# Kernel optimization log

Measured on AMD Instinct MI355X. Metric: run time of the kernel, lower is better.

The kernel has to match this reference:

```python
import jax, jax.numpy as jnp
import numpy as np

B, T, C = 2, 4096, 512
P, PS, CS, MB, FD = 64, 16, 5, 128, 128


def setup_inputs() -> dict:
    key = jax.random.key(0)
    ks = jax.random.split(key, 9)
    y = jax.random.normal(ks[0], (B, T, C), jnp.float32)
    # per-timestep random patch indices into the sequence axis, sorted per patch
    patches = jnp.sort(jax.random.randint(ks[1], (T, P, PS), 0, T), axis=-1).astype(jnp.int32)
    patches_proj = jax.random.randint(ks[2], (T, P), 0, T).astype(jnp.int32)
    W_BASE = jax.random.normal(ks[3], (P, PS, CS), jnp.float32) * 0.05
    W_BIAS = jax.random.normal(ks[4], (P,), jnp.float32) * 0.05
    W_proj2 = jax.random.normal(ks[5], (C, MB), jnp.float32) * (1.0 / np.sqrt(C).astype(np.float32))
    W_proj_comp = jax.random.normal(ks[6], (C, CS), jnp.float32) * (1.0 / np.sqrt(C).astype(np.float32))
    W_presoftmax1 = jax.random.normal(ks[7], (P, P), jnp.float32) * (1.0 / np.sqrt(P).astype(np.float32))
    W_FINAL = jax.random.normal(ks[8], (MB, FD), jnp.float32) * (1.0 / np.sqrt(MB).astype(np.float32))
    return {
        'y': y,
        'W_BASE': W_BASE,
        'W_BIAS': W_BIAS,
        'W_proj2': W_proj2,
        'W_proj_comp': W_proj_comp,
        'W_presoftmax1': W_presoftmax1,
        'W_FINAL': W_FINAL,
        'patches': patches,
        'patches_proj': patches_proj,
    }


def reference(y, W_BASE, W_BIAS, W_proj2, W_proj_comp, W_presoftmax1, W_FINAL, patches, patches_proj):
    # value branch: project then gather one sequence element per (t, patch)
    bm = jnp.einsum('btc,cm->btm', y, W_proj2)          # [B,T,MB]
    mbg = bm[:, patches_proj, :]                        # [B,T,P,MB]  (MBMB)
    # score branch: compress, gather PS elements per (t, patch), weighted reduce
    yc = jnp.einsum('btc,ck->btk', y, W_proj_comp)      # [B,T,CS]
    g = yc[:, patches, :]                               # [B,T,P,PS,CS]
    res = jnp.einsum('btpsc,psc->btp', g, W_BASE) + W_BIAS   # [B,T,P]
    mix = jnp.einsum('btp,pq->btq', res, W_presoftmax1)      # [B,T,P] (no softmax in source)
    out = jnp.einsum('btp,btpm->btm', mix, mbg)              # [B,T,MB]
    return jnp.einsum('btm,mf->btf', out, W_FINAL)           # [B,T,FD]
```

## Files before the change

### kernel.cpp

```cpp
#include <hip/hip_runtime.h>
#include <hip/hip_bf16.h>

#define B_ 2
#define T_ 4096
#define C_ 512
#define P_ 64
#define PS_ 16
#define CS_ 5
#define MB_ 128
#define FD_ 128

using f32x4 = __attribute__((ext_vector_type(4))) float;
using s16x8 = __attribute__((ext_vector_type(8))) short;

static __device__ __forceinline__ float bf_lo(unsigned u) {
  return __uint_as_float(u << 16);
}
static __device__ __forceinline__ float bf_hi(unsigned u) {
  return __uint_as_float(u & 0xffff0000u);
}
static __device__ __forceinline__ float rdlane_f(float v, int p) {
  return __uint_as_float((unsigned)__builtin_amdgcn_readlane((int)__float_as_uint(v), p));
}
static __device__ __forceinline__ ushort bf16u(float f) {
  unsigned x = __float_as_uint(f);
  unsigned r = (x + 0x7fffu + ((x >> 16) & 1u)) >> 16;
  return (ushort)r;
}

__global__ __launch_bounds__(256) void k_cvt(const float* __restrict__ y,
                                             const float* __restrict__ Wc,
                                             ushort* __restrict__ ybf,
                                             ushort* __restrict__ ycp) {
  const int lane = threadIdx.x & 63;
  const int wid  = threadIdx.x >> 6;
  float wc[40];
  {
    const float4* src = (const float4*)(Wc + lane * 40);
    #pragma unroll
    for (int j = 0; j < 10; j++) {
      float4 v = src[j];
      wc[j*4+0] = v.x; wc[j*4+1] = v.y; wc[j*4+2] = v.z; wc[j*4+3] = v.w;
    }
  }
  const int row_base = (blockIdx.x * 4 + wid) * 8;
  #pragma unroll 2
  for (int r = 0; r < 8; r++) {
    const int row = row_base + r;
    const float4* yr = (const float4*)(y + (size_t)row * C_ + lane * 8);
    float4 a = yr[0], b4 = yr[1];
    float e[8] = {a.x, a.y, a.z, a.w, b4.x, b4.y, b4.z, b4.w};
    union { ushort us[8]; uint4 q; } pk;
    #pragma unroll
    for (int j = 0; j < 8; j++) pk.us[j] = bf16u(e[j]);
    *(uint4*)(ybf + (size_t)row * C_ + lane * 8) = pk.q;
    float s0 = 0.f, s1 = 0.f, s2 = 0.f, s3 = 0.f, s4 = 0.f;
    #pragma unroll
    for (int j = 0; j < 8; j++) {
      s0 = fmaf(e[j], wc[j*5+0], s0);
      s1 = fmaf(e[j], wc[j*5+1], s1);
      s2 = fmaf(e[j], wc[j*5+2], s2);
      s3 = fmaf(e[j], wc[j*5+3], s3);
      s4 = fmaf(e[j], wc[j*5+4], s4);
    }
    #pragma unroll
    for (int off = 1; off < 64; off <<= 1) {
      s0 += __shfl_xor(s0, off); s1 += __shfl_xor(s1, off);
      s2 += __shfl_xor(s2, off); s3 += __shfl_xor(s3, off);
      s4 += __shfl_xor(s4, off);
    }
    float myv = (lane == 0) ? s0 : (lane == 1) ? s1 : (lane == 2) ? s2
              : (lane == 3) ? s3 : (lane == 4) ? s4 : 0.f;
    if (lane < 8) ycp[(size_t)row * 8 + lane] = bf16u(myv);
  }
}

__global__ __launch_bounds__(256) void k_cvtW(const float* __restrict__ Wp2,
                                              const float* __restrict__ WF,
                                              ushort* __restrict__ Wp2T,
                                              ushort* __restrict__ WFT) {
  const int id = blockIdx.x * 256 + threadIdx.x;
  if (id < C_ * MB_) {
    const int c = id >> 7, m = id & 127;
    Wp2T[(size_t)m * C_ + c] = bf16u(Wp2[id]);
  }
  const int id2 = id - C_ * MB_;
  if (id2 >= 0 && id2 < MB_ * FD_) {
    const int m = id2 >> 7, f = id2 & 127;
    WFT[(size_t)f * MB_ + m] = bf16u(WF[id2]);
  }
}

template<int KTOT, bool OUTBF>
__global__ __launch_bounds__(256) void k_gemm(const ushort* __restrict__ A,
                                              const ushort* __restrict__ Bt,
                                              void* __restrict__ Cout) {
  __shared__ __align__(16) char smem[(64 + 128) * 128];
  const int tid  = threadIdx.x;
  const int lane = tid & 63;
  const int wid  = tid >> 6;
  const int wm = wid >> 1, wn = wid & 1;
  const int rowA0 = blockIdx.x * 64;

  f32x4 acc[2][4];
  #pragma unroll
  for (int m = 0; m < 2; m++)
    #pragma unroll
    for (int n = 0; n < 4; n++) acc[m][n] = (f32x4){0.f, 0.f, 0.f, 0.f};

  for (int step = 0; step < KTOT / 64; step++) {
    const int kc = step * 64;
    uint4 ra[2], rb[4];
    #pragma unroll
    for (int i = 0; i < 2; i++) {
      const int slot = tid + i * 256, r = slot >> 3, sl = slot & 7;
      ra[i] = *(const uint4*)(A + (size_t)(rowA0 + r) * KTOT + kc + sl * 8);
    }
    #pragma unroll
    for (int i = 0; i < 4; i++) {
      const int slot = tid + i * 256, r = slot >> 3, sl = slot & 7;
      rb[i] = *(const uint4*)(Bt + (size_t)r * KTOT + kc + sl * 8);
    }
    __syncthreads();
    #pragma unroll
    for (int i = 0; i < 2; i++) {
      const int slot = tid + i * 256, r = slot >> 3, sl = slot & 7;
      *(uint4*)(smem + r * 128 + ((sl * 16) ^ ((r & 7) << 4))) = ra[i];
    }
    #pragma unroll
    for (int i = 0; i < 4; i++) {
      const int slot = tid + i * 256, r = slot >> 3, sl = slot & 7;
      *(uint4*)(smem + 8192 + r * 128 + ((sl * 16) ^ ((r & 7) << 4))) = rb[i];
    }
    __syncthreads();
    #pragma unroll
    for (int kk = 0; kk < 2; kk++) {
      const int cb = kk * 64 + (lane >> 4) * 16;
      s16x8 a[2], b[4];
      #pragma unroll
      for (int m = 0; m < 2; m++) {
        const int r = wm * 32 + m * 16 + (lane & 15);
        a[m] = *(const s16x8*)(smem + r * 128 + (cb ^ ((r & 7) << 4)));
      }
      #pragma unroll
      for (int n = 0; n < 4; n++) {
        const int rn = wn * 64 + n * 16 + (lane & 15);
        b[n] = *(const s16x8*)(smem + 8192 + rn * 128 + (cb ^ ((rn & 7) << 4)));
      }
      #pragma unroll
      for (int m = 0; m < 2; m++)
        #pragma unroll
        for (int n = 0; n < 4; n++)
          acc[m][n] = __builtin_amdgcn_mfma_f32_16x16x32_bf16(a[m], b[n], acc[m][n], 0, 0, 0);
    }
  }
  #pragma unroll
  for (int m = 0; m < 2; m++) {
    #pragma unroll
    for (int n = 0; n < 4; n++) {
      #pragma unroll
      for (int reg = 0; reg < 4; reg++) {
        const int grow = rowA0 + wm * 32 + m * 16 + (lane >> 4) * 4 + reg;
        const int gcol = wn * 64 + n * 16 + (lane & 15);
        if (OUTBF)
          ((ushort*)Cout)[(size_t)grow * 128 + gcol] = bf16u(acc[m][n][reg]);
        else
          ((float*)Cout)[(size_t)grow * 128 + gcol] = acc[m][n][reg];
      }
    }
  }
}

__global__ __launch_bounds__(256, 2) void k_mid(
    const ushort* __restrict__ ycp,
    const ushort* __restrict__ bmb,
    const float* __restrict__ WB,
    const float* __restrict__ Wbias,
    const float* __restrict__ Wps1,
    const int* __restrict__ patches,
    const int* __restrict__ pproj,
    ushort* __restrict__ obmb)
{
  const int lane = threadIdx.x & 63;
  const int wid  = threadIdx.x >> 6;
  const int gw   = blockIdx.x * 4 + wid;

  float wb[80];
  {
    const float4* src = (const float4*)(WB + lane * 80);
    #pragma unroll
    for (int j = 0; j < 20; j++) {
      float4 v = src[j];
      wb[j*4+0] = v.x; wb[j*4+1] = v.y; wb[j*4+2] = v.z; wb[j*4+3] = v.w;
    }
  }
  const float bias = Wbias[lane];
  float wcol[64];
  #pragma unroll
  for (int p = 0; p < 64; p++) wcol[p] = Wps1[p * 64 + lane];

  #pragma unroll 1
  for (int tt = 0; tt < 2; tt++) {
    const int t = gw * 2 + tt;
    int idx[16];
    {
      const int4* psrc = (const int4*)(patches + (size_t)t * P_ * PS_ + lane * PS_);
      #pragma unroll
      for (int j = 0; j < 4; j++) {
        int4 v = psrc[j];
        idx[j*4+0] = v.x; idx[j*4+1] = v.y; idx[j*4+2] = v.z; idx[j*4+3] = v.w;
      }
    }
    const int pp = pproj[(size_t)t * P_ + lane];

    #pragma unroll 1
    for (int b = 0; b < B_; b++) {
      const ushort* yb = ycp + (size_t)b * T_ * 8;
      float sum = bias;
      #pragma unroll
      for (int s = 0; s < 16; s++) {
        uint4 g = *(const uint4*)(yb + (size_t)idx[s] * 8);
        sum = fmaf(bf_lo(g.x), wb[s*5+0], sum);
        sum = fmaf(bf_hi(g.x), wb[s*5+1], sum);
        sum = fmaf(bf_lo(g.y), wb[s*5+2], sum);
        sum = fmaf(bf_hi(g.y), wb[s*5+3], sum);
        sum = fmaf(bf_lo(g.z), wb[s*5+4], sum);
      }
      float mix = 0.f;
      #pragma unroll
      for (int p = 0; p < 64; p++)
        mix = fmaf(rdlane_f(sum, p), wcol[p], mix);
      const ushort* bb = bmb + (size_t)b * T_ * MB_;
      float ox = 0.f, oy = 0.f;
      #pragma unroll
      for (int p = 0; p < 64; p++) {
        const float mp = rdlane_f(mix, p);
        const int row = __builtin_amdgcn_readlane(pp, p);
        unsigned v = *(const unsigned*)(bb + (size_t)row * MB_ + lane * 2);
        ox = fmaf(bf_lo(v), mp, ox);
        oy = fmaf(bf_hi(v), mp, oy);
      }
      unsigned pkd = (unsigned)bf16u(ox) | ((unsigned)bf16u(oy) << 16);
      *(unsigned*)(obmb + ((size_t)b * T_ + t) * MB_ + lane * 2) = pkd;
    }
  }
}

extern "C" void kernel_launch(void* const* d_in, const int* in_sizes, int n_in,
                              void* d_out, int out_size, void* d_ws, size_t ws_size,
                              hipStream_t stream) {
  const float* y     = (const float*)d_in[0];
  const float* WB    = (const float*)d_in[1];
  const float* Wbias = (const float*)d_in[2];
  const float* Wp2   = (const float*)d_in[3];
  const float* Wpc   = (const float*)d_in[4];
  const float* Wps1  = (const float*)d_in[5];
  const float* WF    = (const float*)d_in[6];
  const int* patches = (const int*)d_in[7];
  const int* pproj   = (const int*)d_in[8];
  float* out = (float*)d_out;

  char* ws = (char*)d_ws;
  ushort* ybf  = (ushort*)(ws);
  ushort* obmb = (ushort*)(ws);
  ushort* bmb  = (ushort*)(ws + 8388608);
  ushort* ycp  = (ushort*)(ws + 10485760);
  ushort* Wp2T = (ushort*)(ws + 10616832);
  ushort* WFT  = (ushort*)(ws + 10747904);

  k_cvtW<<<dim3(320), dim3(256), 0, stream>>>(Wp2, WF, Wp2T, WFT);
  k_cvt <<<dim3(256), dim3(256), 0, stream>>>(y, Wpc, ybf, ycp);
  k_gemm<512, true> <<<dim3(128), dim3(256), 0, stream>>>(ybf, Wp2T, (void*)bmb);
  k_mid <<<dim3(512), dim3(256), 0, stream>>>(ycp, bmb, WB, Wbias, Wps1,
                                              patches, pproj, obmb);
  k_gemm<128, false><<<dim3(128), dim3(256), 0, stream>>>(obmb, WFT, (void*)out);
}
```

Measured before the change: 151.1 us.

## Fuse weight conversion into prep kernel, convert y inside GEMM, shrink GEMM tiles

Merges the weight-conversion kernel into the y-compression kernel, dropping one launch. The bf16 copy of y is no longer written; the first GEMM reads fp32 y and converts it in registers. Both GEMMs now use 32x64 tiles over 512 blocks instead of 64x128 over 128 blocks, to fill more CUs. In the middle kernel, W_BASE is stored as bf16 and the serial FMA chains are split into multiple accumulators for more ILP. The costs are that every column block reads and converts y again, and W_BASE now carries bf16 precision loss.

```diff
diff --git a/kernel.cpp b/kernel.cpp
--- a/kernel.cpp
+++ b/kernel.cpp
@@ -28,12 +28,35 @@
   return (ushort)r;
 }
 
-__global__ __launch_bounds__(256) void k_cvt(const float* __restrict__ y,
-                                             const float* __restrict__ Wc,
-                                             ushort* __restrict__ ybf,
-                                             ushort* __restrict__ ycp) {
-  const int lane = threadIdx.x & 63;
-  const int wid  = threadIdx.x >> 6;
+__global__ __launch_bounds__(256) void k_prep(const float* __restrict__ y,
+                                              const float* __restrict__ Wc,
+                                              const float* __restrict__ Wp2,
+                                              const float* __restrict__ WF,
+                                              const float* __restrict__ WB,
+                                              ushort* __restrict__ ycp,
+                                              ushort* __restrict__ Wp2T,
+                                              ushort* __restrict__ WFT,
+                                              ushort* __restrict__ WBb) {
+  const int bx = blockIdx.x;
+  const int tid = threadIdx.x;
+  if (bx >= 256) {
+    for (int id = (bx - 256) * 256 + tid; id < 87040; id += 64 * 256) {
+      if (id < 65536) {
+        const int c = id >> 7, m = id & 127;
+        Wp2T[(size_t)m * C_ + c] = bf16u(Wp2[id]);
+      } else if (id < 81920) {
+        const int i2 = id - 65536;
+        const int m = i2 >> 7, f = i2 & 127;
+        WFT[(size_t)f * MB_ + m] = bf16u(WF[i2]);
+      } else {
+        const int i3 = id - 81920;
+        WBb[i3] = bf16u(WB[i3]);
+      }
+    }
+    return;
+  }
+  const int lane = tid & 63;
+  const int wid  = tid >> 6;
   float wc[40];
   {
     const float4* src = (const float4*)(Wc + lane * 40);
@@ -43,17 +66,13 @@
       wc[j*4+0] = v.x; wc[j*4+1] = v.y; wc[j*4+2] = v.z; wc[j*4+3] = v.w;
     }
   }
-  const int row_base = (blockIdx.x * 4 + wid) * 8;
+  const int row_base = (bx * 4 + wid) * 8;
   #pragma unroll 2
   for (int r = 0; r < 8; r++) {
     const int row = row_base + r;
     const float4* yr = (const float4*)(y + (size_t)row * C_ + lane * 8);
     float4 a = yr[0], b4 = yr[1];
     float e[8] = {a.x, a.y, a.z, a.w, b4.x, b4.y, b4.z, b4.w};
-    union { ushort us[8]; uint4 q; } pk;
-    #pragma unroll
-    for (int j = 0; j < 8; j++) pk.us[j] = bf16u(e[j]);
-    *(uint4*)(ybf + (size_t)row * C_ + lane * 8) = pk.q;
     float s0 = 0.f, s1 = 0.f, s2 = 0.f, s3 = 0.f, s4 = 0.f;
     #pragma unroll
     for (int j = 0; j < 8; j++) {
@@ -75,98 +94,82 @@
   }
 }
 
-__global__ __launch_bounds__(256) void k_cvtW(const float* __restrict__ Wp2,
-                                              const float* __restrict__ WF,
-                                              ushort* __restrict__ Wp2T,
-                                              ushort* __restrict__ WFT) {
-  const int id = blockIdx.x * 256 + threadIdx.x;
-  if (id < C_ * MB_) {
-    const int c = id >> 7, m = id & 127;
-    Wp2T[(size_t)m * C_ + c] = bf16u(Wp2[id]);
-  }
-  const int id2 = id - C_ * MB_;
-  if (id2 >= 0 && id2 < MB_ * FD_) {
-    const int m = id2 >> 7, f = id2 & 127;
-    WFT[(size_t)f * MB_ + m] = bf16u(WF[id2]);
-  }
-}
-
-template<int KTOT, bool OUTBF>
-__global__ __launch_bounds__(256) void k_gemm(const ushort* __restrict__ A,
+template<int KTOT, bool OUTBF, bool A_F32>
+__global__ __launch_bounds__(256) void k_gemm(const void* __restrict__ Asrc,
                                               const ushort* __restrict__ Bt,
                                               void* __restrict__ Cout) {
-  __shared__ __align__(16) char smem[(64 + 128) * 128];
+  __shared__ __align__(16) char smem[(32 + 64) * 128];
   const int tid  = threadIdx.x;
   const int lane = tid & 63;
   const int wid  = tid >> 6;
   const int wm = wid >> 1, wn = wid & 1;
-  const int rowA0 = blockIdx.x * 64;
-
-  f32x4 acc[2][4];
-  #pragma unroll
-  for (int m = 0; m < 2; m++)
-    #pragma unroll
-    for (int n = 0; n < 4; n++) acc[m][n] = (f32x4){0.f, 0.f, 0.f, 0.f};
+  const int rowA0 = (blockIdx.x >> 1) * 32;
+  const int bn    = blockIdx.x & 1;
+
+  f32x4 acc[2];
+  acc[0] = (f32x4){0.f, 0.f, 0.f, 0.f};
+  acc[1] = (f32x4){0.f, 0.f, 0.f, 0.f};
 
   for (int step = 0; step < KTOT / 64; step++) {
     const int kc = step * 64;
-    uint4 ra[2], rb[4];
+    uint4 ra;
+    {
+      const int r = tid >> 3, sl = tid & 7;
+      if (A_F32) {
+        const float4* ap = (const float4*)((const float*)Asrc +
+                            (size_t)(rowA0 + r) * KTOT + kc + sl * 8);
+        float4 f0 = ap[0], f1 = ap[1];
+        union { ushort us[8]; uint4 q; } pk;
+        pk.us[0] = bf16u(f0.x); pk.us[1] = bf16u(f0.y);
+        pk.us[2] = bf16u(f0.z); pk.us[3] = bf16u(f0.w);
+        pk.us[4] = bf16u(f1.x); pk.us[5] = bf16u(f1.y);
+        pk.us[6] = bf16u(f1.z); pk.us[7] = bf16u(f1.w);
+        ra = pk.q;
+      } else {
+        ra = *(const uint4*)((const ushort*)Asrc +
+                             (size_t)(rowA0 + r) * KTOT + kc + sl * 8);
+      }
+    }
+    uint4 rb[2];
     #pragma unroll
     for (int i = 0; i < 2; i++) {
       const int slot = tid + i * 256, r = slot >> 3, sl = slot & 7;
-      ra[i] = *(const uint4*)(A + (size_t)(rowA0 + r) * KTOT + kc + sl * 8);
-    }
-    #pragma unroll
-    for (int i = 0; i < 4; i++) {
-      const int slot = tid + i * 256, r = slot >> 3, sl = slot & 7;
-      rb[i] = *(const uint4*)(Bt + (size_t)r * KTOT + kc + sl * 8);
+      rb[i] = *(const uint4*)(Bt + (size_t)(bn * 64 + r) * KTOT + kc + sl * 8);
     }
     __syncthreads();
+    {
+      const int r = tid >> 3, sl = tid & 7;
+      *(uint4*)(smem + r * 128 + ((sl * 16) ^ ((r & 7) << 4))) = ra;
+    }
     #pragma unroll
     for (int i = 0; i < 2; i++) {
       const int slot = tid + i * 256, r = slot >> 3, sl = slot & 7;
-      *(uint4*)(smem + r * 128 + ((sl * 16) ^ ((r & 7) << 4))) = ra[i];
-    }
-    #pragma unroll
-    for (int i = 0; i < 4; i++) {
-      const int slot = tid + i * 256, r = slot >> 3, sl = slot & 7;
-      *(uint4*)(smem + 8192 + r * 128 + ((sl * 16) ^ ((r & 7) << 4))) = rb[i];
+      *(uint4*)(smem + 4096 + r * 128 + ((sl * 16) ^ ((r & 7) << 4))) = rb[i];
     }
     __syncthreads();
     #pragma unroll
     for (int kk = 0; kk < 2; kk++) {
       const int cb = kk * 64 + (lane >> 4) * 16;
-      s16x8 a[2], b[4];
-      #pragma unroll
-      for (int m = 0; m < 2; m++) {
-        const int r = wm * 32 + m * 16 + (lane & 15);
-        a[m] = *(const s16x8*)(smem + r * 128 + (cb ^ ((r & 7) << 4)));
-      }
-      #pragma unroll
-      for (int n = 0; n < 4; n++) {
-        const int rn = wn * 64 + n * 16 + (lane & 15);
-        b[n] = *(const s16x8*)(smem + 8192 + rn * 128 + (cb ^ ((rn & 7) << 4)));
-      }
-      #pragma unroll
-      for (int m = 0; m < 2; m++)
-        #pragma unroll
-        for (int n = 0; n < 4; n++)
-          acc[m][n] = __builtin_amdgcn_mfma_f32_16x16x32_bf16(a[m], b[n], acc[m][n], 0, 0, 0);
+      const int r = wm * 16 + (lane & 15);
+      s16x8 a = *(const s16x8*)(smem + r * 128 + (cb ^ ((r & 7) << 4)));
+      #pragma unroll
+      for (int n = 0; n < 2; n++) {
+        const int rn = wn * 32 + n * 16 + (lane & 15);
+        s16x8 b = *(const s16x8*)(smem + 4096 + rn * 128 + (cb ^ ((rn & 7) << 4)));
+        acc[n] = __builtin_amdgcn_mfma_f32_16x16x32_bf16(a, b, acc[n], 0, 0, 0);
+      }
     }
   }
   #pragma unroll
-  for (int m = 0; m < 2; m++) {
-    #pragma unroll
-    for (int n = 0; n < 4; n++) {
-      #pragma unroll
-      for (int reg = 0; reg < 4; reg++) {
-        const int grow = rowA0 + wm * 32 + m * 16 + (lane >> 4) * 4 + reg;
-        const int gcol = wn * 64 + n * 16 + (lane & 15);
-        if (OUTBF)
-          ((ushort*)Cout)[(size_t)grow * 128 + gcol] = bf16u(acc[m][n][reg]);
-        else
-          ((float*)Cout)[(size_t)grow * 128 + gcol] = acc[m][n][reg];
-      }
+  for (int n = 0; n < 2; n++) {
+    #pragma unroll
+    for (int reg = 0; reg < 4; reg++) {
+      const int grow = rowA0 + wm * 16 + (lane >> 4) * 4 + reg;
+      const int gcol = bn * 64 + wn * 32 + n * 16 + (lane & 15);
+      if (OUTBF)
+        ((ushort*)Cout)[(size_t)grow * 128 + gcol] = bf16u(acc[n][reg]);
+      else
+        ((float*)Cout)[(size_t)grow * 128 + gcol] = acc[n][reg];
     }
   }
 }
@@ -174,7 +177,7 @@
 __global__ __launch_bounds__(256, 2) void k_mid(
     const ushort* __restrict__ ycp,
     const ushort* __restrict__ bmb,
-    const float* __restrict__ WB,
+    const ushort* __restrict__ WBb,
     const float* __restrict__ Wbias,
     const float* __restrict__ Wps1,
     const int* __restrict__ patches,
@@ -185,14 +188,11 @@
   const int wid  = threadIdx.x >> 6;
   const int gw   = blockIdx.x * 4 + wid;
 
-  float wb[80];
+  union { unsigned u[40]; uint4 q[10]; } wbu;
   {
-    const float4* src = (const float4*)(WB + lane * 80);
-    #pragma unroll
-    for (int j = 0; j < 20; j++) {
-      float4 v = src[j];
-      wb[j*4+0] = v.x; wb[j*4+1] = v.y; wb[j*4+2] = v.z; wb[j*4+3] = v.w;
-    }
+    const uint4* src = (const uint4*)(WBb + lane * 80);
+    #pragma unroll
+    for (int j = 0; j < 10; j++) wbu.q[j] = src[j];
   }
   const float bias = Wbias[lane];
   float wcol[64];
@@ -216,31 +216,48 @@
     #pragma unroll 1
     for (int b = 0; b < B_; b++) {
       const ushort* yb = ycp + (size_t)b * T_ * 8;
-      float sum = bias;
+      float c0 = bias, c1 = 0.f, c2 = 0.f, c3 = 0.f, c4 = 0.f;
       #pragma unroll
       for (int s = 0; s < 16; s++) {
         uint4 g = *(const uint4*)(yb + (size_t)idx[s] * 8);
-        sum = fmaf(bf_lo(g.x), wb[s*5+0], sum);
-        sum = fmaf(bf_hi(g.x), wb[s*5+1], sum);
-        sum = fmaf(bf_lo(g.y), wb[s*5+2], sum);
-        sum = fmaf(bf_hi(g.y), wb[s*5+3], sum);
-        sum = fmaf(bf_lo(g.z), wb[s*5+4], sum);
-      }
-      float mix = 0.f;
-      #pragma unroll
-      for (int p = 0; p < 64; p++)
-        mix = fmaf(rdlane_f(sum, p), wcol[p], mix);
+        const int e = s * 5;
+        const float w0 = ((e+0)&1) ? bf_hi(wbu.u[(e+0)>>1]) : bf_lo(wbu.u[(e+0)>>1]);
+        const float w1 = ((e+1)&1) ? bf_hi(wbu.u[(e+1)>>1]) : bf_lo(wbu.u[(e+1)>>1]);
+        const float w2 = ((e+2)&1) ? bf_hi(wbu.u[(e+2)>>1]) : bf_lo(wbu.u[(e+2)>>1]);
+        const float w3 = ((e+3)&1) ? bf_hi(wbu.u[(e+3)>>1]) : bf_lo(wbu.u[(e+3)>>1]);
+        const float w4 = ((e+4)&1) ? bf_hi(wbu.u[(e+4)>>1]) : bf_lo(wbu.u[(e+4)>>1]);
+        c0 = fmaf(bf_lo(g.x), w0, c0);
+        c1 = fmaf(bf_hi(g.x), w1, c1);
+        c2 = fmaf(bf_lo(g.y), w2, c2);
+        c3 = fmaf(bf_hi(g.y), w3, c3);
+        c4 = fmaf(bf_lo(g.z), w4, c4);
+      }
+      const float sum = (c0 + c1) + (c2 + c3) + c4;
+      float m0 = 0.f, m1 = 0.f, m2 = 0.f, m3 = 0.f;
+      #pragma unroll
+      for (int p = 0; p < 64; p += 4) {
+        m0 = fmaf(rdlane_f(sum, p + 0), wcol[p + 0], m0);
+        m1 = fmaf(rdlane_f(sum, p + 1), wcol[p + 1], m1);
+        m2 = fmaf(rdlane_f(sum, p + 2), wcol[p + 2], m2);
+        m3 = fmaf(rdlane_f(sum, p + 3), wcol[p + 3], m3);
+      }
+      const float mix = (m0 + m1) + (m2 + m3);
       const ushort* bb = bmb + (size_t)b * T_ * MB_;
-      float ox = 0.f, oy = 0.f;
-      #pragma unroll
-      for (int p = 0; p < 64; p++) {
-        const float mp = rdlane_f(mix, p);
-        const int row = __builtin_amdgcn_readlane(pp, p);
-        unsigned v = *(const unsigned*)(bb + (size_t)row * MB_ + lane * 2);
-        ox = fmaf(bf_lo(v), mp, ox);
-        oy = fmaf(bf_hi(v), mp, oy);
-      }
-      unsigned pkd = (unsigned)bf16u(ox) | ((unsigned)bf16u(oy) << 16);
+      float oxa = 0.f, oya = 0.f, oxb = 0.f, oyb = 0.f;
+      #pragma unroll
+      for (int p = 0; p < 64; p += 2) {
+        const float mpa = rdlane_f(mix, p);
+        const int rowa = __builtin_amdgcn_readlane(pp, p);
+        unsigned va = *(const unsigned*)(bb + (size_t)rowa * MB_ + lane * 2);
+        oxa = fmaf(bf_lo(va), mpa, oxa);
+        oya = fmaf(bf_hi(va), mpa, oya);
+        const float mpb = rdlane_f(mix, p + 1);
+        const int rowb = __builtin_amdgcn_readlane(pp, p + 1);
+        unsigned vb = *(const unsigned*)(bb + (size_t)rowb * MB_ + lane * 2);
+        oxb = fmaf(bf_lo(vb), mpb, oxb);
+        oyb = fmaf(bf_hi(vb), mpb, oyb);
+      }
+      unsigned pkd = (unsigned)bf16u(oxa + oxb) | ((unsigned)bf16u(oya + oyb) << 16);
       *(unsigned*)(obmb + ((size_t)b * T_ + t) * MB_ + lane * 2) = pkd;
     }
   }
@@ -261,17 +278,17 @@
   float* out = (float*)d_out;
 
   char* ws = (char*)d_ws;
-  ushort* ybf  = (ushort*)(ws);
-  ushort* obmb = (ushort*)(ws);
-  ushort* bmb  = (ushort*)(ws + 8388608);
-  ushort* ycp  = (ushort*)(ws + 10485760);
-  ushort* Wp2T = (ushort*)(ws + 10616832);
-  ushort* WFT  = (ushort*)(ws + 10747904);
-
-  k_cvtW<<<dim3(320), dim3(256), 0, stream>>>(Wp2, WF, Wp2T, WFT);
-  k_cvt <<<dim3(256), dim3(256), 0, stream>>>(y, Wpc, ybf, ycp);
-  k_gemm<512, true> <<<dim3(128), dim3(256), 0, stream>>>(ybf, Wp2T, (void*)bmb);
-  k_mid <<<dim3(512), dim3(256), 0, stream>>>(ycp, bmb, WB, Wbias, Wps1,
+  ushort* bmb  = (ushort*)(ws);
+  ushort* obmb = (ushort*)(ws + 2097152);
+  ushort* ycp  = (ushort*)(ws + 4194304);
+  ushort* Wp2T = (ushort*)(ws + 4325376);
+  ushort* WFT  = (ushort*)(ws + 4456448);
+  ushort* WBb  = (ushort*)(ws + 4489216);
+
+  k_prep<<<dim3(320), dim3(256), 0, stream>>>(y, Wpc, Wp2, WF, WB,
+                                              ycp, Wp2T, WFT, WBb);
+  k_gemm<512, true,  true ><<<dim3(512), dim3(256), 0, stream>>>((const void*)y, Wp2T, (void*)bmb);
+  k_mid <<<dim3(512), dim3(256), 0, stream>>>(ycp, bmb, WBb, Wbias, Wps1,
                                               patches, pproj, obmb);
-  k_gemm<128, false><<<dim3(128), dim3(256), 0, stream>>>(obmb, WFT, (void*)out);
-}
+  k_gemm<128, false, false><<<dim3(512), dim3(256), 0, stream>>>((const void*)obmb, WFT, (void*)out);
+}
```

Measured after the change: 186.8 us. 23.6% more time.
